# Performance work log

Hardware: AMD Instinct MI355X
Metric: run time of the kernel (lower is better)

Reference implementation:

```python
import jax, jax.numpy as jnp
import numpy as np

B, S, D, H = 2, 2048, 1024, 16
HD = D // H  # head_dim = 64


def setup_inputs() -> dict:
    key = jax.random.key(0)
    ks = jax.random.split(key, 5)
    scale = 0.02
    x = jax.random.normal(ks[0], (B, S, D), dtype=jnp.float32)
    Wq = scale * jax.random.normal(ks[1], (H, D, HD), dtype=jnp.float32)
    Wk = scale * jax.random.normal(ks[2], (H, D, HD), dtype=jnp.float32)
    Wv = scale * jax.random.normal(ks[3], (H, D, HD), dtype=jnp.float32)
    Wo = scale * jax.random.normal(ks[4], (D, D), dtype=jnp.float32)
    bq = jnp.zeros((H, HD), dtype=jnp.float32)
    bk = jnp.zeros((H, HD), dtype=jnp.float32)
    bv = jnp.zeros((H, HD), dtype=jnp.float32)
    bo = jnp.zeros((D,), dtype=jnp.float32)
    return {"x": x, "Wq": Wq, "bq": bq, "Wk": Wk, "bk": bk,
            "Wv": Wv, "bv": bv, "Wo": Wo, "bo": bo}


def reference(x, Wq, bq, Wk, bk, Wv, bv, Wo, bo):
    # Per-head QKV projections (the torch module's per-head nn.Linear list,
    # vectorized over the head axis h). Dropout is identity (eval mode).
    q = jnp.einsum("bsd,hde->bhse", x, Wq) + bq[None, :, None, :]  # [B,H,S,HD]
    k = jnp.einsum("bsd,hde->bhse", x, Wk) + bk[None, :, None, :]
    v = jnp.einsum("bsd,hde->bhse", x, Wv) + bv[None, :, None, :]

    norm = jnp.asarray(np.sqrt(HD), dtype=x.dtype)
    scores = jnp.einsum("bhse,bhte->bhst", q, k) / norm  # [B,H,S,S]
    causal = jnp.tril(jnp.ones((S, S), dtype=bool))
    scores = jnp.where(causal[None, None], scores, jnp.asarray(-jnp.inf, dtype=scores.dtype))
    attn = jax.nn.softmax(scores, axis=-1)

    wv = jnp.einsum("bhst,bhte->bhse", attn, v)          # [B,H,S,HD]
    wv = jnp.transpose(wv, (0, 2, 1, 3)).reshape(B, S, D)  # concat heads on last dim
    out = wv @ Wo.T + bo                                   # output projection
    return out
```

## Files before the change

### kernel.cpp

```cpp
#include <hip/hip_runtime.h>


#define DD 1024
#define SS 2048
#define BB 2
#define HH 16
#define HD 64
#define QSCALE 0.18033688011112042f
#define LSTR 88

typedef __attribute__((ext_vector_type(8))) short short8;
typedef __attribute__((ext_vector_type(4))) float float4v;
typedef unsigned short ushort;
typedef unsigned int uint;

__device__ inline ushort f2bf(float f) {
    union { float f; uint i; } v; v.f = f;
    uint r = v.i + 0x7FFF + ((v.i >> 16) & 1);
    return (ushort)(r >> 16);
}
#if __has_builtin(__builtin_amdgcn_cvt_pk_bf16_f32)
typedef __bf16 bf16x2 __attribute__((ext_vector_type(2)));
__device__ inline uint pack_bf2(float a, float b) {
    union { bf16x2 v; uint u; } c;
    c.v = __builtin_amdgcn_cvt_pk_bf16_f32(a, b);
    return c.u;
}
#else
__device__ inline uint pack_bf2(float a, float b) {
    union { float f; uint i; } x, y; x.f = a; y.f = b;
    return ((x.i + 0x8000u) >> 16) | (((y.i + 0x8000u) >> 16) << 16);
}
#endif

__device__ __forceinline__ void cp16(const ushort* g, ushort* l) {
    __builtin_amdgcn_global_load_lds((const __attribute__((address_space(1))) void*)g,
                                     (__attribute__((address_space(3))) void*)l,
                                     16, 0, 0);
}

__global__ __launch_bounds__(256) void prep(const float* __restrict__ x,
                                            const float* __restrict__ Wo,
                                            const float* __restrict__ Wq,
                                            const float* __restrict__ Wk,
                                            const float* __restrict__ Wv,
                                            ushort* __restrict__ xb,
                                            ushort* __restrict__ Wob,
                                            ushort* __restrict__ W3T) {
    __shared__ ushort T[64][65];
    int bid = blockIdx.x, t = threadIdx.x;
    if (bid < 5120) {
        const float* src; ushort* dst; int j;
        if (bid < 4096) { src = x;  dst = xb;  j = bid * 256 + t; }
        else            { src = Wo; dst = Wob; j = (bid - 4096) * 256 + t; }
        float4 v = ((const float4*)src)[j];
        ushort o[4] = { f2bf(v.x), f2bf(v.y), f2bf(v.z), f2bf(v.w) };
        ((uint2*)dst)[j] = *(const uint2*)o;
        return;
    }
    int i = bid - 5120;
    int z = i >> 8, h = (i >> 4) & 15, d0 = (i & 15) * 64;
    const float* W = z == 0 ? Wq : (z == 1 ? Wk : Wv);
    const float* Wh = W + h * DD * HD;
    ushort* Wt = W3T + ((size_t)z * HH + h) * HD * DD;
    #pragma unroll
    for (int s = 0; s < 4; s++) {
        int idx = t + s * 256;
        int d = idx >> 4, e4 = (idx & 15) * 4;
        float4 v = *(const float4*)(Wh + (d0 + d) * HD + e4);
        T[d][e4 + 0] = f2bf(v.x); T[d][e4 + 1] = f2bf(v.y);
        T[d][e4 + 2] = f2bf(v.z); T[d][e4 + 3] = f2bf(v.w);
    }
    __syncthreads();
    #pragma unroll
    for (int s = 0; s < 2; s++) {
        int idx = t + s * 256;
        int e = idx >> 3, d8 = (idx & 7) * 8;
        ushort tmp[8];
        #pragma unroll
        for (int j = 0; j < 8; j++) tmp[j] = T[d8 + j][e];
        *(uint4*)(Wt + e * DD + d0 + d8) = *(uint4*)tmp;
    }
}

__global__ __launch_bounds__(256) void gemm_qkv(const ushort* __restrict__ xb,
                                                const ushort* __restrict__ W3T,
                                                const float* __restrict__ bq,
                                                const float* __restrict__ bk,
                                                const float* __restrict__ bv,
                                                ushort* __restrict__ qb,
                                                ushort* __restrict__ kb,
                                                ushort* __restrict__ vT) {
    __shared__ ushort Al[128 * 64];
    __shared__ ushort Bl[3][64 * 64];
    int m0 = blockIdx.x * 128, n0 = blockIdx.y * 64;
    int t = threadIdx.x, lane = t & 63, w = t >> 6;
    int wm = w & 1, wn = w >> 1;
    int qm = lane >> 4, lm = lane & 15;

    const ushort* W0 = W3T + (size_t)n0 * DD;
    const ushort* W1 = W3T + (size_t)(HH * HD + n0) * DD;
    const ushort* W2 = W3T + (size_t)(2 * HH * HD + n0) * DD;

    float4v acc[3][4][2] = {};
    for (int k0 = 0; k0 < DD; k0 += 64) {
        __syncthreads();
        #pragma unroll
        for (int s = 0; s < 4; s++) {
            int c = t + s * 256;
            int row = c >> 3;
            int j = (c & 7) ^ (row & 7);
            cp16(xb + (size_t)(m0 + row) * DD + k0 + j * 8, Al + c * 8);
        }
        #pragma unroll
        for (int s = 0; s < 2; s++) {
            int c = t + s * 256;
            int row = c >> 3;
            int j = (c & 7) ^ (row & 7);
            cp16(W0 + (size_t)row * DD + k0 + j * 8, Bl[0] + c * 8);
            cp16(W1 + (size_t)row * DD + k0 + j * 8, Bl[1] + c * 8);
            cp16(W2 + (size_t)row * DD + k0 + j * 8, Bl[2] + c * 8);
        }
        __syncthreads();
        #pragma unroll
        for (int h2 = 0; h2 < 2; h2++) {
            int sw = ((((h2 << 2) | qm) ^ (lm & 7)) << 3);
            short8 a[4];
            #pragma unroll
            for (int i = 0; i < 4; i++)
                a[i] = *(const short8*)(Al + ((wm * 64 + i * 16 + lm) << 6) + sw);
            #pragma unroll
            for (int z = 0; z < 3; z++) {
                short8 b0 = *(const short8*)(Bl[z] + ((wn * 32 + lm) << 6) + sw);
                short8 b1 = *(const short8*)(Bl[z] + ((wn * 32 + 16 + lm) << 6) + sw);
                if (z == 2) {
                    #pragma unroll
                    for (int i = 0; i < 4; i++) {
                        acc[2][i][0] = __builtin_amdgcn_mfma_f32_16x16x32_bf16(a[i], b0, acc[2][i][0], 0, 0, 0);
                        acc[2][i][1] = __builtin_amdgcn_mfma_f32_16x16x32_bf16(a[i], b1, acc[2][i][1], 0, 0, 0);
                    }
                } else {
                    #pragma unroll
                    for (int i = 0; i < 4; i++) {
                        acc[z][i][0] = __builtin_amdgcn_mfma_f32_16x16x32_bf16(b0, a[i], acc[z][i][0], 0, 0, 0);
                        acc[z][i][1] = __builtin_amdgcn_mfma_f32_16x16x32_bf16(b1, a[i], acc[z][i][1], 0, 0, 0);
                    }
                }
            }
        }
    }
    #pragma unroll
    for (int z = 0; z < 2; z++) {
        const float* bias = z == 0 ? bq : bk;
        ushort* Out = z == 0 ? qb : kb;
        float sc = z == 0 ? QSCALE : 1.0f;
        #pragma unroll
        for (int j = 0; j < 2; j++) {
            int nb = n0 + wn * 32 + j * 16 + qm * 4;
            float4 b4 = *(const float4*)(bias + nb);
            #pragma unroll
            for (int i = 0; i < 4; i++) {
                int m = m0 + wm * 64 + i * 16 + lm;
                uint2 o2;
                o2.x = pack_bf2((acc[z][i][j][0] + b4.x) * sc, (acc[z][i][j][1] + b4.y) * sc);
                o2.y = pack_bf2((acc[z][i][j][2] + b4.z) * sc, (acc[z][i][j][3] + b4.w) * sc);
                *(uint2*)(Out + (size_t)m * DD + nb) = o2;
            }
        }
    }
    #pragma unroll
    for (int j = 0; j < 2; j++) {
        int n = n0 + wn * 32 + j * 16 + lm;
        int h = n >> 6, e = n & 63;
        float bb = bv[n];
        #pragma unroll
        for (int i = 0; i < 4; i++) {
            int m = m0 + wm * 64 + i * 16 + qm * 4;
            int b_ = m >> 11, s = m & (SS - 1);
            uint2 o2;
            o2.x = pack_bf2(acc[2][i][j][0] + bb, acc[2][i][j][1] + bb);
            o2.y = pack_bf2(acc[2][i][j][2] + bb, acc[2][i][j][3] + bb);
            *(uint2*)(vT + ((size_t)(b_ * HH + h) * HD + e) * SS + s) = o2;
        }
    }
}

__global__ __launch_bounds__(512, 4) void attn(const ushort* __restrict__ Q,
                                               const ushort* __restrict__ K,
                                               const ushort* __restrict__ VT,
                                               ushort* __restrict__ O) {
    __shared__ ushort QP[128][LSTR];
    __shared__ ushort Kl[2][64 * 64];
    __shared__ ushort Vl[2][64 * 64];
    int id = blockIdx.x;
    int bh = id & 31;
    int j5 = (id >> 5) & 7;
    int qt = (id < 256) ? (15 - 2 * j5) : (2 * j5);
    int b = bh >> 4, h = bh & 15;
    int m0 = qt * 128;
    int njt = 2 * (qt + 1);
    const ushort* Qp = Q + (size_t)b * SS * DD + h * HD;
    const ushort* Kp = K + (size_t)b * SS * DD + h * HD;
    const ushort* Vp = VT + (size_t)bh * HD * SS;
    int t = threadIdx.x, lane = t & 63, w = t >> 6;
    int qm = lane >> 4, lm = lane & 15;
    int row0 = t >> 3, colc = (t & 7) * 8;
    int srow = t >> 3;
    int sj = (t & 7) ^ (srow & 7);

    *(uint4*)(&QP[row0][colc])      = *(const uint4*)(Qp + (size_t)(m0 + row0) * DD + colc);
    *(uint4*)(&QP[row0 + 64][colc]) = *(const uint4*)(Qp + (size_t)(m0 + row0 + 64) * DD + colc);
    cp16(Kp + (size_t)srow * DD + sj * 8, Kl[0] + t * 8);
    cp16(Vp + (size_t)srow * SS + sj * 8, Vl[0] + t * 8);
    __syncthreads();

    short8 qf[2];
    qf[0] = *(const short8*)(&QP[w * 16 + lm][qm * 8]);
    qf[1] = *(const short8*)(&QP[w * 16 + lm][32 + qm * 8]);

    float4v o[4] = {};
    float li = 0.f;
    int cur = 0;
    int qg = m0 + w * 16 + lm;
    int swz = ((qm ^ (lm & 7)) << 3);
    int swz1 = (((4 | qm) ^ (lm & 7)) << 3);

    for (int jt = 0; jt < njt; jt++) {
        if (jt) __syncthreads();
        if (jt + 1 < njt) {
            int nn = (jt + 1) * 64;
            cp16(Kp + (size_t)(nn + srow) * DD + sj * 8, Kl[cur ^ 1] + t * 8);
            cp16(Vp + (size_t)srow * SS + nn + sj * 8, Vl[cur ^ 1] + t * 8);
        }

        float4v s[4] = {};
        #pragma unroll
        for (int j = 0; j < 4; j++) {
            short8 ak0 = *(const short8*)(Kl[cur] + ((j * 16 + lm) << 6) + swz);
            short8 ak1 = *(const short8*)(Kl[cur] + ((j * 16 + lm) << 6) + swz1);
            s[j] = __builtin_amdgcn_mfma_f32_16x16x32_bf16(ak0, qf[0], s[j], 0, 0, 0);
            s[j] = __builtin_amdgcn_mfma_f32_16x16x32_bf16(ak1, qf[1], s[j], 0, 0, 0);
        }
        if (jt >= 2 * qt) {
            #pragma unroll
            for (int j = 0; j < 4; j++)
                #pragma unroll
                for (int r = 0; r < 4; r++)
                    if (jt * 64 + j * 16 + qm * 4 + r > qg) s[j][r] = -__builtin_inff();
        }
        #pragma unroll
        for (int j = 0; j < 4; j++) {
            float p0 = __builtin_amdgcn_exp2f(s[j][0]);
            float p1 = __builtin_amdgcn_exp2f(s[j][1]);
            float p2 = __builtin_amdgcn_exp2f(s[j][2]);
            float p3 = __builtin_amdgcn_exp2f(s[j][3]);
            li += (p0 + p1) + (p2 + p3);
            uint2 u; u.x = pack_bf2(p0, p1); u.y = pack_bf2(p2, p3);
            *(uint2*)(&QP[w * 16 + lm][j * 16 + qm * 4]) = u;
        }
        asm volatile("s_waitcnt lgkmcnt(0)" ::: "memory");

        #pragma unroll
        for (int kc = 0; kc < 2; kc++) {
            short8 ap = *(const short8*)(&QP[w * 16 + lm][kc * 32 + qm * 8]);
            int so = kc ? swz1 : swz;
            #pragma unroll
            for (int jn = 0; jn < 4; jn++) {
                short8 av = *(const short8*)(Vl[cur] + ((jn * 16 + lm) << 6) + so);
                o[jn] = __builtin_amdgcn_mfma_f32_16x16x32_bf16(av, ap, o[jn], 0, 0, 0);
            }
        }
        cur ^= 1;
    }
    li += __shfl_xor(li, 16, 64);
    li += __shfl_xor(li, 32, 64);
    float inv = 1.f / li;
    ushort* Ob = O + ((size_t)b * SS + qg) * DD + h * HD;
    #pragma unroll
    for (int jn = 0; jn < 4; jn++) {
        uint2 u;
        u.x = pack_bf2(o[jn][0] * inv, o[jn][1] * inv);
        u.y = pack_bf2(o[jn][2] * inv, o[jn][3] * inv);
        *(uint2*)(Ob + jn * 16 + qm * 4) = u;
    }
}

__global__ __launch_bounds__(256) void gemm_out(const ushort* __restrict__ X,
                                                const ushort* __restrict__ Wob,
                                                const float* __restrict__ bo,
                                                float* __restrict__ Out) {
    __shared__ ushort Al[128 * 64];
    __shared__ ushort Bl[64 * 64];
    int m0 = blockIdx.x * 128, n0 = blockIdx.y * 64;
    int t = threadIdx.x, lane = t & 63, w = t >> 6;
    int wm = w & 1, wn = w >> 1;
    int qm = lane >> 4, lm = lane & 15;

    float4v acc[4][2] = {};
    for (int k0 = 0; k0 < DD; k0 += 64) {
        __syncthreads();
        #pragma unroll
        for (int s = 0; s < 4; s++) {
            int c = t + s * 256;
            int row = c >> 3;
            int j = (c & 7) ^ (row & 7);
            cp16(X + (size_t)(m0 + row) * DD + k0 + j * 8, Al + c * 8);
        }
        #pragma unroll
        for (int s = 0; s < 2; s++) {
            int c = t + s * 256;
            int row = c >> 3;
            int j = (c & 7) ^ (row & 7);
            cp16(Wob + (size_t)(n0 + row) * DD + k0 + j * 8, Bl + c * 8);
        }
        __syncthreads();
        #pragma unroll
        for (int h2 = 0; h2 < 2; h2++) {
            int sw = ((((h2 << 2) | qm) ^ (lm & 7)) << 3);
            short8 a[4], b[2];
            #pragma unroll
            for (int i = 0; i < 4; i++)
                a[i] = *(const short8*)(Al + ((wm * 64 + i * 16 + lm) << 6) + sw);
            #pragma unroll
            for (int j = 0; j < 2; j++)
                b[j] = *(const short8*)(Bl + ((wn * 32 + j * 16 + lm) << 6) + sw);
            #pragma unroll
            for (int i = 0; i < 4; i++)
                #pragma unroll
                for (int j = 0; j < 2; j++)
                    acc[i][j] = __builtin_amdgcn_mfma_f32_16x16x32_bf16(b[j], a[i], acc[i][j], 0, 0, 0);
        }
    }
    #pragma unroll
    for (int j = 0; j < 2; j++) {
        int nb = n0 + wn * 32 + j * 16 + qm * 4;
        float4 b4 = *(const float4*)(bo + nb);
        #pragma unroll
        for (int i = 0; i < 4; i++) {
            int m = m0 + wm * 64 + i * 16 + lm;
            float4 st;
            st.x = acc[i][j][0] + b4.x;
            st.y = acc[i][j][1] + b4.y;
            st.z = acc[i][j][2] + b4.z;
            st.w = acc[i][j][3] + b4.w;
            *(float4*)(Out + (size_t)m * DD + nb) = st;
        }
    }
}

extern "C" void kernel_launch(void* const* d_in, const int* in_sizes, int n_in,
                              void* d_out, int out_size, void* d_ws, size_t ws_size,
                              hipStream_t stream) {
    const float* x   = (const float*)d_in[0];
    const float* Wq  = (const float*)d_in[1];
    const float* bq  = (const float*)d_in[2];
    const float* Wk  = (const float*)d_in[3];
    const float* bk  = (const float*)d_in[4];
    const float* Wv_ = (const float*)d_in[5];
    const float* bv  = (const float*)d_in[6];
    const float* Wo  = (const float*)d_in[7];
    const float* bo  = (const float*)d_in[8];
    float* out = (float*)d_out;

    ushort* xb  = (ushort*)d_ws;
    ushort* W3T = xb  + (size_t)BB * SS * DD;
    ushort* Wob = W3T + (size_t)3 * HH * HD * DD;
    ushort* qb  = Wob + (size_t)DD * DD;
    ushort* kb  = qb + (size_t)BB * SS * DD;
    ushort* vT  = kb + (size_t)BB * SS * DD;
    ushort* wvb = vT + (size_t)BB * SS * DD;

    prep<<<dim3(5888), 256, 0, stream>>>(x, Wo, Wq, Wk, Wv_, xb, Wob, W3T);
    gemm_qkv<<<dim3(32, 16), 256, 0, stream>>>(xb, W3T, bq, bk, bv, qb, kb, vT);
    attn<<<dim3(512), 512, 0, stream>>>(qb, kb, vT, wvb);
    gemm_out<<<dim3(32, 16), 256, 0, stream>>>(wvb, Wob, bo, out);
}
```

Baseline: 182.3 us.

## Shrink attention blocks to 64 query rows with swizzled Q/P tile and priorities

The attention kernel now uses 256-thread blocks covering 64 query rows instead of 512 threads over 128 rows, launching 1024 blocks in a four-way load-balanced causal order. The Q tile is loaded asynchronously into a swizzled 64x64 buffer that also holds P, replacing the padded 128x88 array. MFMA sections are bracketed with s_setprio to favour matrix work across waves. The intent is better CU occupancy and load balance plus fewer LDS bank conflicts, at the cost of reloading each K/V tile for twice as many blocks.

```diff
diff --git a/kernel.cpp b/kernel.cpp
--- a/kernel.cpp
+++ b/kernel.cpp
@@ -7,7 +7,6 @@
 #define HH 16
 #define HD 64
 #define QSCALE 0.18033688011112042f
-#define LSTR 88
 
 typedef __attribute__((ext_vector_type(8))) short short8;
 typedef __attribute__((ext_vector_type(4))) float float4v;
@@ -185,55 +184,63 @@
     }
 }
 
-__global__ __launch_bounds__(512, 4) void attn(const ushort* __restrict__ Q,
+__global__ __launch_bounds__(256, 4) void attn(const ushort* __restrict__ Q,
                                                const ushort* __restrict__ K,
                                                const ushort* __restrict__ VT,
                                                ushort* __restrict__ O) {
-    __shared__ ushort QP[128][LSTR];
+    __shared__ ushort Ql[64 * 64];
     __shared__ ushort Kl[2][64 * 64];
     __shared__ ushort Vl[2][64 * 64];
     int id = blockIdx.x;
     int bh = id & 31;
     int j5 = (id >> 5) & 7;
-    int qt = (id < 256) ? (15 - 2 * j5) : (2 * j5);
+    int quad = id >> 8;
+    int qt = (quad == 0) ? (31 - j5) : (quad == 1) ? (16 + j5)
+           : (quad == 2) ? (15 - j5) : j5;
     int b = bh >> 4, h = bh & 15;
-    int m0 = qt * 128;
-    int njt = 2 * (qt + 1);
+    int m0 = qt * 64;
     const ushort* Qp = Q + (size_t)b * SS * DD + h * HD;
     const ushort* Kp = K + (size_t)b * SS * DD + h * HD;
     const ushort* Vp = VT + (size_t)bh * HD * SS;
     int t = threadIdx.x, lane = t & 63, w = t >> 6;
     int qm = lane >> 4, lm = lane & 15;
-    int row0 = t >> 3, colc = (t & 7) * 8;
-    int srow = t >> 3;
-    int sj = (t & 7) ^ (srow & 7);
-
-    *(uint4*)(&QP[row0][colc])      = *(const uint4*)(Qp + (size_t)(m0 + row0) * DD + colc);
-    *(uint4*)(&QP[row0 + 64][colc]) = *(const uint4*)(Qp + (size_t)(m0 + row0 + 64) * DD + colc);
-    cp16(Kp + (size_t)srow * DD + sj * 8, Kl[0] + t * 8);
-    cp16(Vp + (size_t)srow * SS + sj * 8, Vl[0] + t * 8);
+    int qg = m0 + w * 16 + lm;
+    int swz = ((qm ^ (lm & 7)) << 3);
+    int swz1 = (((4 | qm) ^ (lm & 7)) << 3);
+
+    #pragma unroll
+    for (int s2 = 0; s2 < 2; s2++) {
+        int c = t + s2 * 256;
+        int row = c >> 3, sj = (c & 7) ^ (row & 7);
+        cp16(Qp + (size_t)(m0 + row) * DD + sj * 8, Ql + c * 8);
+        cp16(Kp + (size_t)row * DD + sj * 8, Kl[0] + c * 8);
+        cp16(Vp + (size_t)row * SS + sj * 8, Vl[0] + c * 8);
+    }
     __syncthreads();
 
     short8 qf[2];
-    qf[0] = *(const short8*)(&QP[w * 16 + lm][qm * 8]);
-    qf[1] = *(const short8*)(&QP[w * 16 + lm][32 + qm * 8]);
+    qf[0] = *(const short8*)(Ql + ((w * 16 + lm) << 6) + swz);
+    qf[1] = *(const short8*)(Ql + ((w * 16 + lm) << 6) + swz1);
 
     float4v o[4] = {};
     float li = 0.f;
     int cur = 0;
-    int qg = m0 + w * 16 + lm;
-    int swz = ((qm ^ (lm & 7)) << 3);
-    int swz1 = (((4 | qm) ^ (lm & 7)) << 3);
-
-    for (int jt = 0; jt < njt; jt++) {
+
+    for (int jt = 0; jt <= qt; jt++) {
         if (jt) __syncthreads();
-        if (jt + 1 < njt) {
+        if (jt < qt) {
             int nn = (jt + 1) * 64;
-            cp16(Kp + (size_t)(nn + srow) * DD + sj * 8, Kl[cur ^ 1] + t * 8);
-            cp16(Vp + (size_t)srow * SS + nn + sj * 8, Vl[cur ^ 1] + t * 8);
+            #pragma unroll
+            for (int s2 = 0; s2 < 2; s2++) {
+                int c = t + s2 * 256;
+                int row = c >> 3, sj = (c & 7) ^ (row & 7);
+                cp16(Kp + (size_t)(nn + row) * DD + sj * 8, Kl[cur ^ 1] + c * 8);
+                cp16(Vp + (size_t)row * SS + nn + sj * 8, Vl[cur ^ 1] + c * 8);
+            }
         }
 
         float4v s[4] = {};
+        __builtin_amdgcn_s_setprio(1);
         #pragma unroll
         for (int j = 0; j < 4; j++) {
             short8 ak0 = *(const short8*)(Kl[cur] + ((j * 16 + lm) << 6) + swz);
@@ -241,7 +248,8 @@
             s[j] = __builtin_amdgcn_mfma_f32_16x16x32_bf16(ak0, qf[0], s[j], 0, 0, 0);
             s[j] = __builtin_amdgcn_mfma_f32_16x16x32_bf16(ak1, qf[1], s[j], 0, 0, 0);
         }
-        if (jt >= 2 * qt) {
+        __builtin_amdgcn_s_setprio(0);
+        if (jt == qt) {
             #pragma unroll
             for (int j = 0; j < 4; j++)
                 #pragma unroll
@@ -256,20 +264,22 @@
             float p3 = __builtin_amdgcn_exp2f(s[j][3]);
             li += (p0 + p1) + (p2 + p3);
             uint2 u; u.x = pack_bf2(p0, p1); u.y = pack_bf2(p2, p3);
-            *(uint2*)(&QP[w * 16 + lm][j * 16 + qm * 4]) = u;
+            int pc = (2 * j + (qm >> 1)) ^ (lm & 7);
+            *(uint2*)(Ql + ((w * 16 + lm) << 6) + (pc << 3) + (qm & 1) * 4) = u;
         }
         asm volatile("s_waitcnt lgkmcnt(0)" ::: "memory");
 
+        __builtin_amdgcn_s_setprio(1);
         #pragma unroll
         for (int kc = 0; kc < 2; kc++) {
-            short8 ap = *(const short8*)(&QP[w * 16 + lm][kc * 32 + qm * 8]);
-            int so = kc ? swz1 : swz;
+            short8 ap = *(const short8*)(Ql + ((w * 16 + lm) << 6) + (kc ? swz1 : swz));
             #pragma unroll
             for (int jn = 0; jn < 4; jn++) {
-                short8 av = *(const short8*)(Vl[cur] + ((jn * 16 + lm) << 6) + so);
+                short8 av = *(const short8*)(Vl[cur] + ((jn * 16 + lm) << 6) + (kc ? swz1 : swz));
                 o[jn] = __builtin_amdgcn_mfma_f32_16x16x32_bf16(av, ap, o[jn], 0, 0, 0);
             }
         }
+        __builtin_amdgcn_s_setprio(0);
         cur ^= 1;
     }
     li += __shfl_xor(li, 16, 64);
@@ -372,6 +382,6 @@
 
     prep<<<dim3(5888), 256, 0, stream>>>(x, Wo, Wq, Wk, Wv_, xb, Wob, W3T);
     gemm_qkv<<<dim3(32, 16), 256, 0, stream>>>(xb, W3T, bq, bk, bv, qb, kb, vT);
-    attn<<<dim3(512), 512, 0, stream>>>(qb, kb, vT, wvb);
+    attn<<<dim3(1024), 256, 0, stream>>>(qb, kb, vT, wvb);
     gemm_out<<<dim3(32, 16), 256, 0, stream>>>(wvb, Wob, bo, out);
 }
```

After: 181.3 us. About the same (-0.5%).
